# Kernel optimization log

Measured on AMD Instinct MI355X. Metric: run time of the kernel, lower is better.

The kernel has to match this reference:

```python
import jax, jax.numpy as jnp
import numpy as np

DIM = 128
B, N = 4, 4096


def setup_inputs() -> dict:
    key = jax.random.key(0)
    k1, k2, k3 = jax.random.split(key, 3)
    return {
        "key": jax.random.normal(k1, (B, N, DIM), dtype=jnp.float32),
        "query": jax.random.normal(k2, (B, N, DIM), dtype=jnp.float32),
        "value": jax.random.normal(k3, (B, N, DIM), dtype=jnp.float32),
    }


def reference(key, query, value):
    # score[b, i, j] = <query[b, i], key[b, j]> / sqrt(dim)
    inv_sqrt_dim = 1.0 / jnp.sqrt(jnp.float32(DIM))
    score = jnp.einsum("bqd,bkd->bqk", query, key) * inv_sqrt_dim
    attn = jax.nn.softmax(score, axis=-1)
    context = jnp.einsum("bqk,bkd->bqd", attn, value)
    return (context, attn)
```

## Files before the change

kernel.cpp:

```cpp
#include <hip/hip_runtime.h>
#include <hip/hip_bf16.h>

#define BDIM 4
#define NSEQ 4096
#define DHEAD 128
#define SCALE 0.08838834764831845f

typedef __bf16 bf16x8 __attribute__((ext_vector_type(8)));
typedef float f32x4 __attribute__((ext_vector_type(4)));
typedef float f32x16 __attribute__((ext_vector_type(16)));
typedef unsigned int u32x4 __attribute__((ext_vector_type(4)));

__device__ __forceinline__ unsigned short f2bf(float f){
    return __builtin_bit_cast(unsigned short, (__bf16)f);
}
__device__ __forceinline__ unsigned long long pack4(float4 u){
    return (unsigned long long)f2bf(u.x)
         | ((unsigned long long)f2bf(u.y) << 16)
         | ((unsigned long long)f2bf(u.z) << 32)
         | ((unsigned long long)f2bf(u.w) << 48);
}
__device__ __forceinline__ void gload_lds16(const void* g, void* l){
    __builtin_amdgcn_global_load_lds(
        (const __attribute__((address_space(1))) unsigned int*)g,
        (__attribute__((address_space(3))) unsigned int*)l, 16, 0, 0);
}

extern "C" __global__ __launch_bounds__(256, 4)
void attn_stats(const float* __restrict__ K, const float* __restrict__ Q,
                float* __restrict__ pbase, int pstride)
{
    __shared__ __align__(16) char Klds[64 * 256];

    const int bid = blockIdx.x;
    const int ks  = bid & 3;
    const int rt  = (bid >> 2) & 63;
    const int b   = bid >> 8;
    const int tid = threadIdx.x;
    const int lane = tid & 63;
    const int w    = tid >> 6;
    const int g    = lane >> 4;
    const int c    = lane & 15;
    const int rowbase = rt * 64;

    const float* qrow = Q + ((size_t)b * NSEQ + rowbase + w * 16 + c) * DHEAD;
    bf16x8 qf[4];
#pragma unroll
    for (int kk = 0; kk < 4; kk++) {
        const float4* p0 = (const float4*)(qrow + g * 8 + kk * 32);
        float4 u = p0[0], v = p0[1];
        bf16x8 t;
        t[0] = (__bf16)(u.x * SCALE); t[1] = (__bf16)(u.y * SCALE);
        t[2] = (__bf16)(u.z * SCALE); t[3] = (__bf16)(u.w * SCALE);
        t[4] = (__bf16)(v.x * SCALE); t[5] = (__bf16)(v.y * SCALE);
        t[6] = (__bf16)(v.z * SCALE); t[7] = (__bf16)(v.w * SCALE);
        qf[kk] = t;
    }

    float m[4], l[4];
#pragma unroll
    for (int r = 0; r < 4; r++) { m[r] = -1e30f; l[r] = 0.0f; }

    const int f  = tid & 31;
    const int r0 = tid >> 5;

    for (int kt = 0; kt < 16; kt++) {
        const float* ktile = K + ((size_t)b * NSEQ + ks * 1024 + kt * 64) * DHEAD;
#pragma unroll
        for (int i = 0; i < 8; i++) {
            int r = r0 + i * 8;
            float4 u = *(const float4*)(ktile + (size_t)r * DHEAD + f * 4);
            *(unsigned long long*)(Klds + r * 256 + ((f * 8) ^ ((r & 7) << 4))) = pack4(u);
        }
        __syncthreads();

        f32x4 acc[4];
#pragma unroll
        for (int n = 0; n < 4; n++) acc[n] = (f32x4){0.f, 0.f, 0.f, 0.f};
#pragma unroll
        for (int n = 0; n < 4; n++) {
            int row = n * 16 + c;
#pragma unroll
            for (int kk = 0; kk < 4; kk++) {
                bf16x8 kf = *(const bf16x8*)(Klds + row * 256 +
                                ((g * 16 + kk * 64) ^ ((row & 7) << 4)));
                acc[n] = __builtin_amdgcn_mfma_f32_16x16x32_bf16(qf[kk], kf, acc[n], 0, 0, 0);
            }
        }

#pragma unroll
        for (int r = 0; r < 4; r++) {
            float t = fmaxf(fmaxf(acc[0][r], acc[1][r]), fmaxf(acc[2][r], acc[3][r]));
            t = fmaxf(t, __shfl_xor(t, 1));
            t = fmaxf(t, __shfl_xor(t, 2));
            t = fmaxf(t, __shfl_xor(t, 4));
            t = fmaxf(t, __shfl_xor(t, 8));
            float mn = fmaxf(m[r], t);
            float sc = __expf(m[r] - mn);
            float ps = __expf(acc[0][r] - mn) + __expf(acc[1][r] - mn)
                     + __expf(acc[2][r] - mn) + __expf(acc[3][r] - mn);
            ps += __shfl_xor(ps, 1);
            ps += __shfl_xor(ps, 2);
            ps += __shfl_xor(ps, 4);
            ps += __shfl_xor(ps, 8);
            l[r] = l[r] * sc + ps;
            m[r] = mn;
        }
        __syncthreads();
    }

    if (c == 0) {
#pragma unroll
        for (int r = 0; r < 4; r++) {
            size_t row = rowbase + w * 16 + g * 4 + r;
            float* p = pbase + ((size_t)b * NSEQ + row) * pstride + ks * 2;
            p[0] = m[r];
            p[1] = l[r];
        }
    }
}

extern "C" __global__ __launch_bounds__(256, 4)
void repack3(const float* __restrict__ K, const float* __restrict__ V,
             char* __restrict__ ws)
{
    const int bid = blockIdx.x;
    const int T = bid & 127;
    const int b = bid >> 7;
    const int tid = threadIdx.x;

    char* Kp = ws + ((size_t)(b * 128 + T) << 14);
    const float* Ks = K + ((size_t)b * NSEQ + T * 32) * DHEAD;
    const float* Vs = V + ((size_t)b * NSEQ + T * 32) * DHEAD;

#pragma unroll
    for (int i = 0; i < 2; i++) {
        int u = tid + 256 * i;
        int ds = u >> 6, ln = u & 63;
        int m = ln & 31, hi = ln >> 5;
        const float* s = Ks + (size_t)m * DHEAD + ds * 16 + hi * 8;
        float4 a = *(const float4*)s;
        float4 bq = *(const float4*)(s + 4);
        ulonglong2 wv;
        wv.x = pack4(a);
        wv.y = pack4(bq);
        *(ulonglong2*)(Kp + u * 16) = wv;
    }
#pragma unroll
    for (int i = 0; i < 2; i++) {
        int u = tid + 256 * i;
        int f = u >> 6, ln = u & 63;
        int dg = f >> 1, kb = f & 1;
        int dd = ln & 31, hi = ln >> 5;
        int d = dg * 32 + dd;
        const float* s = Vs + (size_t)(kb * 16 + hi * 8) * DHEAD + d;
        float v0 = s[0 * DHEAD], v1 = s[1 * DHEAD], v2 = s[2 * DHEAD], v3 = s[3 * DHEAD];
        float v4 = s[4 * DHEAD], v5 = s[5 * DHEAD], v6 = s[6 * DHEAD], v7 = s[7 * DHEAD];
        ulonglong2 wv;
        wv.x = (unsigned long long)f2bf(v0)
             | ((unsigned long long)f2bf(v1) << 16)
             | ((unsigned long long)f2bf(v2) << 32)
             | ((unsigned long long)f2bf(v3) << 48);
        wv.y = (unsigned long long)f2bf(v4)
             | ((unsigned long long)f2bf(v5) << 16)
             | ((unsigned long long)f2bf(v6) << 32)
             | ((unsigned long long)f2bf(v7) << 48);
        *(ulonglong2*)(Kp + 8192 + u * 16) = wv;
    }
}

extern "C" __global__ __launch_bounds__(256, 2)
void attn_mf(const char* __restrict__ ws, const float* __restrict__ Q,
             float* __restrict__ out, float* __restrict__ part, int use_atomic)
{
    __shared__ __align__(16) char LDS[32768];

    const int bid = blockIdx.x;
    const int ks  = bid & 3;
    const int qt  = (bid >> 2) & 31;
    const int b   = bid >> 7;
    const int tid = threadIdx.x;
    const int wv  = tid >> 6;
    const int lane = tid & 63;
    const int hi   = lane >> 5;
    const int qq   = lane & 31;
    const int q    = qt * 128 + wv * 32 + qq;

    float* attn = out + (size_t)BDIM * NSEQ * DHEAD;
    const float* pb = (const float*)(ws + (8u << 20));

    float Cq;
    {
        const float* prow = pb + ((size_t)b * NSEQ + q) * 8;
        float4 p0 = *(const float4*)prow;
        float4 p1 = *(const float4*)(prow + 4);
        float M = fmaxf(fmaxf(p0.x, p0.z), fmaxf(p1.x, p1.z));
        float L = p0.y * __expf(p0.x - M) + p0.w * __expf(p0.z - M)
                + p1.y * __expf(p1.x - M) + p1.w * __expf(p1.z - M);
        Cq = M + __logf(L);
    }

    const float* qrow = Q + ((size_t)b * NSEQ + q) * DHEAD;
    bf16x8 qf[8];
#pragma unroll
    for (int ds = 0; ds < 8; ds++) {
        const float4* p0 = (const float4*)(qrow + ds * 16 + hi * 8);
        float4 u = p0[0], v = p0[1];
        bf16x8 t;
        t[0] = (__bf16)(u.x * SCALE); t[1] = (__bf16)(u.y * SCALE);
        t[2] = (__bf16)(u.z * SCALE); t[3] = (__bf16)(u.w * SCALE);
        t[4] = (__bf16)(v.x * SCALE); t[5] = (__bf16)(v.y * SCALE);
        t[6] = (__bf16)(v.z * SCALE); t[7] = (__bf16)(v.w * SCALE);
        qf[ds] = t;
    }

    f32x16 ctx[4];
#pragma unroll
    for (int dg = 0; dg < 4; dg++) ctx[dg] = (f32x16)(0.0f);

    const char* img = ws + ((size_t)(b * 128 + ks * 32) << 14);

#pragma unroll
    for (int i = 0; i < 4; i++) {
        int o = tid * 16 + i * 4096;
        gload_lds16(img + o, LDS + o);
    }

    float* arowb = attn + ((size_t)b * NSEQ + q) * NSEQ + ks * 1024 + 4 * hi;

    for (int kt = 0; kt < 32; kt++) {
        __builtin_amdgcn_s_barrier();
        __builtin_amdgcn_sched_barrier(0);
        if (kt < 31) {
            const char* src = img + ((size_t)(kt + 1) << 14);
            char* dst = LDS + (((kt + 1) & 1) << 14);
#pragma unroll
            for (int i = 0; i < 4; i++) {
                int o = tid * 16 + i * 4096;
                gload_lds16(src + o, dst + o);
            }
            asm volatile("s_waitcnt vmcnt(4)" ::: "memory");
        } else {
            asm volatile("s_waitcnt vmcnt(0)" ::: "memory");
        }
        __builtin_amdgcn_s_barrier();
        __builtin_amdgcn_sched_barrier(0);

        const char* bufc = LDS + ((kt & 1) << 14);

        f32x16 sacc = (f32x16)(0.0f);
        __builtin_amdgcn_s_setprio(1);
#pragma unroll
        for (int ds = 0; ds < 8; ds++) {
            bf16x8 kf = *(const bf16x8*)(bufc + ds * 1024 + lane * 16);
            sacc = __builtin_amdgcn_mfma_f32_32x32x16_bf16(kf, qf[ds], sacc, 0, 0, 0);
        }
        __builtin_amdgcn_s_setprio(0);

        float p[16];
#pragma unroll
        for (int r = 0; r < 16; r++) p[r] = __expf(sacc[r] - Cq);

        float* arow = arowb + kt * 32;
#pragma unroll
        for (int j = 0; j < 4; j++) {
            float4 pv = {p[4 * j], p[4 * j + 1], p[4 * j + 2], p[4 * j + 3]};
            *(float4*)(arow + 8 * j) = pv;
        }

        unsigned int bpk[8], sb[8];
#pragma unroll
        for (int i = 0; i < 8; i++)
            bpk[i] = (unsigned int)f2bf(p[2 * i]) | ((unsigned int)f2bf(p[2 * i + 1]) << 16);
#pragma unroll
        for (int i = 0; i < 8; i++)
            sb[i] = (unsigned int)__shfl_xor((int)bpk[i], 32);

        u32x4 w0, w1;
        w0[0] = hi ? sb[2] : bpk[0];
        w0[1] = hi ? sb[3] : bpk[1];
        w0[2] = hi ? bpk[2] : sb[0];
        w0[3] = hi ? bpk[3] : sb[1];
        w1[0] = hi ? sb[6] : bpk[4];
        w1[1] = hi ? sb[7] : bpk[5];
        w1[2] = hi ? bpk[6] : sb[4];
        w1[3] = hi ? bpk[7] : sb[5];
        bf16x8 pf0 = __builtin_bit_cast(bf16x8, w0);
        bf16x8 pf1 = __builtin_bit_cast(bf16x8, w1);

        __builtin_amdgcn_s_setprio(1);
#pragma unroll
        for (int dg = 0; dg < 4; dg++) {
            bf16x8 vf0 = *(const bf16x8*)(bufc + 8192 + (dg * 2 + 0) * 1024 + lane * 16);
            bf16x8 vf1 = *(const bf16x8*)(bufc + 8192 + (dg * 2 + 1) * 1024 + lane * 16);
            ctx[dg] = __builtin_amdgcn_mfma_f32_32x32x16_bf16(vf0, pf0, ctx[dg], 0, 0, 0);
            ctx[dg] = __builtin_amdgcn_mfma_f32_32x32x16_bf16(vf1, pf1, ctx[dg], 0, 0, 0);
        }
        __builtin_amdgcn_s_setprio(0);
    }

    if (!use_atomic) {
        float* cp = part + (((size_t)(ks * 4 + b) * NSEQ + q) * DHEAD) + 4 * hi;
#pragma unroll
        for (int dg = 0; dg < 4; dg++)
#pragma unroll
            for (int j = 0; j < 4; j++) {
                float4 v = {ctx[dg][4 * j], ctx[dg][4 * j + 1],
                            ctx[dg][4 * j + 2], ctx[dg][4 * j + 3]};
                *(float4*)(cp + dg * 32 + 8 * j) = v;
            }
    } else {
        float* cp = out + ((size_t)b * NSEQ + q) * DHEAD + 4 * hi;
#pragma unroll
        for (int dg = 0; dg < 4; dg++)
#pragma unroll
            for (int j = 0; j < 4; j++)
#pragma unroll
                for (int e = 0; e < 4; e++)
                    atomicAdd(cp + dg * 32 + 8 * j + e, ctx[dg][4 * j + e]);
    }
}

extern "C" __global__ __launch_bounds__(256, 4)
void ctx_reduce(const float4* __restrict__ part, float4* __restrict__ out)
{
    const size_t gt = (size_t)blockIdx.x * 256 + threadIdx.x;
    const size_t stride = (size_t)BDIM * NSEQ * DHEAD / 4;
    float4 a = part[gt];
    float4 b = part[gt + stride];
    float4 c = part[gt + 2 * stride];
    float4 d = part[gt + 3 * stride];
    float4 s;
    s.x = (a.x + b.x) + (c.x + d.x);
    s.y = (a.y + b.y) + (c.y + d.y);
    s.z = (a.z + b.z) + (c.z + d.z);
    s.w = (a.w + b.w) + (c.w + d.w);
    out[gt] = s;
}

extern "C" __global__ __launch_bounds__(512, 2)
void attn_final_fb(const float* __restrict__ K, const float* __restrict__ Q,
                   const float* __restrict__ V, float* __restrict__ out)
{
    __shared__ __align__(16) char LDS[81920];

    const int bid = blockIdx.x;
    const int rt  = bid & 63;
    const int b   = bid >> 6;
    const int tid = threadIdx.x;
    const int rowbase = rt * 64;
    const int lane = tid & 63;
    const int w    = tid >> 6;
    const int rw   = w & 3;
    const int grp  = w >> 2;
    const int g    = lane >> 4;
    const int c    = lane & 15;
    const int t    = tid & 255;

    float* ctxOut = out;
    float* attn   = out + (size_t)BDIM * NSEQ * DHEAD;

    char* Klds  = LDS + grp * 16384;
    char* Vtlds = LDS + 32768 + grp * 16384;
    char* Plds  = LDS + 65536 + w * 2048;

    float Cq;
    {
        const float* prow = attn + ((size_t)b * NSEQ + rowbase + rw * 16 + c) * NSEQ;
        float4 p0 = *(const float4*)prow;
        float4 p1 = *(const float4*)(prow + 4);
        float M = fmaxf(fmaxf(p0.x, p0.z), fmaxf(p1.x, p1.z));
        float L = p0.y * __expf(p0.x - M) + p0.w * __expf(p0.z - M)
                + p1.y * __expf(p1.x - M) + p1.w * __expf(p1.z - M);
        Cq = M + __logf(L);
    }

    const float* qrow = Q + ((size_t)b * NSEQ + rowbase + rw * 16 + c) * DHEAD;
    bf16x8 qf[4];
#pragma unroll
    for (int kk = 0; kk < 4; kk++) {
        const float4* p0 = (const float4*)(qrow + g * 8 + kk * 32);
        float4 u = p0[0], v = p0[1];
        bf16x8 tt;
        tt[0] = (__bf16)(u.x * SCALE); tt[1] = (__bf16)(u.y * SCALE);
        tt[2] = (__bf16)(u.z * SCALE); tt[3] = (__bf16)(u.w * SCALE);
        tt[4] = (__bf16)(v.x * SCALE); tt[5] = (__bf16)(v.y * SCALE);
        tt[6] = (__bf16)(v.z * SCALE); tt[7] = (__bf16)(v.w * SCALE);
        qf[kk] = tt;
    }

    f32x4 ctx[8];
#pragma unroll
    for (int n2 = 0; n2 < 8; n2++) ctx[n2] = (f32x4){0.f, 0.f, 0.f, 0.f};

    __syncthreads();

    const int fK = t & 31;
    const int rK = t >> 5;
    const int dq = t & 15;
    const int kb = t >> 4;
    const int k0 = kb * 4;
    const int d0 = dq * 2;

    const float* kbase = K + ((size_t)b * NSEQ + grp * 2048) * DHEAD;
    const float* vbase = V + ((size_t)b * NSEQ + grp * 2048) * DHEAD;

    float4 kreg[8];
    float2 vreg[4][4];

#pragma unroll
    for (int i = 0; i < 8; i++)
        kreg[i] = *(const float4*)(kbase + (size_t)(rK + i * 8) * DHEAD + fK * 4);
#pragma unroll
    for (int i = 0; i < 4; i++)
#pragma unroll
        for (int j = 0; j < 4; j++)
            vreg[i][j] = *(const float2*)(vbase + (size_t)(k0 + j) * DHEAD + d0 + 32 * i);

    for (int kt = 0; kt < 32; kt++) {
        __builtin_amdgcn_s_barrier();

#pragma unroll
        for (int i = 0; i < 8; i++) {
            int row = rK + i * 8;
            *(unsigned long long*)(Klds + row * 256 + ((fK * 8) ^ ((row & 7) << 4))) = pack4(kreg[i]);
        }
#pragma unroll
        for (int i = 0; i < 4; i++) {
            int d = d0 + 32 * i;
            unsigned long long rr0 =
                (unsigned long long)f2bf(vreg[i][0].x)
              | ((unsigned long long)f2bf(vreg[i][1].x) << 16)
              | ((unsigned long long)f2bf(vreg[i][2].x) << 32)
              | ((unsigned long long)f2bf(vreg[i][3].x) << 48);
            unsigned long long rr1 =
                (unsigned long long)f2bf(vreg[i][0].y)
              | ((unsigned long long)f2bf(vreg[i][1].y) << 16)
              | ((unsigned long long)f2bf(vreg[i][2].y) << 32)
              | ((unsigned long long)f2bf(vreg[i][3].y) << 48);
            int swz = (d & 7) << 4;
            *(unsigned long long*)(Vtlds + d * 128 + ((k0 * 2) ^ swz)) = rr0;
            *(unsigned long long*)(Vtlds + (d + 1) * 128 + ((k0 * 2) ^ (swz + 16))) = rr1;
        }
        asm volatile("s_waitcnt lgkmcnt(0)" ::: "memory");
        __builtin_amdgcn_s_barrier();

        {
            int kn = (kt + 1) & 31;
            const float* kp = kbase + (size_t)kn * 64 * DHEAD;
            const float* vp = vbase + (size_t)kn * 64 * DHEAD;
#pragma unroll
            for (int i = 0; i < 8; i++)
                kreg[i] = *(const float4*)(kp + (size_t)(rK + i * 8) * DHEAD + fK * 4);
#pragma unroll
            for (int i = 0; i < 4; i++)
#pragma unroll
                for (int j = 0; j < 4; j++)
                    vreg[i][j] = *(const float2*)(vp + (size_t)(k0 + j) * DHEAD + d0 + 32 * i);
        }

        f32x4 sacc[4];
#pragma unroll
        for (int nt = 0; nt < 4; nt++) sacc[nt] = (f32x4){0.f, 0.f, 0.f, 0.f};
        __builtin_amdgcn_s_setprio(1);
#pragma unroll
        for (int nt = 0; nt < 4; nt++) {
            int row = nt * 16 + c;
#pragma unroll
            for (int kk = 0; kk < 4; kk++) {
                bf16x8 kf = *(const bf16x8*)(Klds + row * 256 +
                                ((g * 16 + kk * 64) ^ ((row & 7) << 4)));
                sacc[nt] = __builtin_amdgcn_mfma_f32_16x16x32_bf16(kf, qf[kk], sacc[nt], 0, 0, 0);
            }
        }
        __builtin_amdgcn_s_setprio(0);

        const int col0 = grp * 2048 + kt * 64;
        float* arow = attn + ((size_t)b * NSEQ + rowbase + rw * 16 + c) * NSEQ + col0;
#pragma unroll
        for (int nt = 0; nt < 4; nt++) {
            float4 pv;
            pv.x = __expf(sacc[nt][0] - Cq);
            pv.y = __expf(sacc[nt][1] - Cq);
            pv.z = __expf(sacc[nt][2] - Cq);
            pv.w = __expf(sacc[nt][3] - Cq);
            *(float4*)(arow + nt * 16 + g * 4) = pv;
            *(unsigned long long*)(Plds + c * 128 +
                ((nt * 32 + g * 8) ^ ((c & 7) << 4))) = pack4(pv);
        }
        asm volatile("s_waitcnt lgkmcnt(0)" ::: "memory");
        __builtin_amdgcn_sched_barrier(0);

        bf16x8 pf[2];
#pragma unroll
        for (int kk = 0; kk < 2; kk++)
            pf[kk] = *(const bf16x8*)(Plds + c * 128 +
                        ((kk * 64 + g * 16) ^ ((c & 7) << 4)));

        __builtin_amdgcn_s_setprio(1);
#pragma unroll
        for (int n2 = 0; n2 < 8; n2++) {
            int d = n2 * 16 + c;
#pragma unroll
            for (int kk = 0; kk < 2; kk++) {
                bf16x8 vff = *(const bf16x8*)(Vtlds + d * 128 +
                                ((kk * 64 + g * 16) ^ ((d & 7) << 4)));
                ctx[n2] = __builtin_amdgcn_mfma_f32_16x16x32_bf16(pf[kk], vff, ctx[n2], 0, 0, 0);
            }
        }
        __builtin_amdgcn_s_setprio(0);
    }

    __syncthreads();

    float* red = (float*)LDS;
    if (grp == 1) {
#pragma unroll
        for (int n2 = 0; n2 < 8; n2++)
#pragma unroll
            for (int r = 0; r < 4; r++)
                red[(rw * 16 + g * 4 + r) * 128 + n2 * 16 + c] = ctx[n2][r];
    }
    __syncthreads();
    if (grp == 0) {
#pragma unroll
        for (int n2 = 0; n2 < 8; n2++)
#pragma unroll
            for (int r = 0; r < 4; r++) {
                size_t row = rowbase + rw * 16 + g * 4 + r;
                ctxOut[((size_t)b * NSEQ + row) * DHEAD + n2 * 16 + c] =
                    ctx[n2][r] + red[(rw * 16 + g * 4 + r) * 128 + n2 * 16 + c];
            }
    }
}

extern "C" void kernel_launch(void* const* d_in, const int* in_sizes, int n_in,
                              void* d_out, int out_size, void* d_ws, size_t ws_size,
                              hipStream_t stream)
{
    const float* K = (const float*)d_in[0];
    const float* Q = (const float*)d_in[1];
    const float* V = (const float*)d_in[2];
    float* out  = (float*)d_out;
    float* attn = out + (size_t)BDIM * NSEQ * DHEAD;

    const size_t ctx_bytes  = (size_t)BDIM * NSEQ * DHEAD * sizeof(float);
    const size_t need_part  = (9u << 20) + 4 * ctx_bytes;
    const size_t need_atom  = (8u << 20) + (size_t)BDIM * NSEQ * 8 * sizeof(float);

    if (ws_size >= need_part) {
        char* ws = (char*)d_ws;
        float* pb = (float*)(ws + (8u << 20));
        float* part = (float*)(ws + (9u << 20));
        attn_stats<<<dim3(4 * 64 * 4), dim3(256), 0, stream>>>(K, Q, pb, 8);
        repack3<<<dim3(4 * 128), dim3(256), 0, stream>>>(K, V, ws);
        attn_mf<<<dim3(512), dim3(256), 0, stream>>>(ws, Q, out, part, 0);
        ctx_reduce<<<dim3(2048), dim3(256), 0, stream>>>((const float4*)part, (float4*)out);
    } else if (ws_size >= need_atom) {
        char* ws = (char*)d_ws;
        float* pb = (float*)(ws + (8u << 20));
        hipMemsetAsync(out, 0, ctx_bytes, stream);
        attn_stats<<<dim3(4 * 64 * 4), dim3(256), 0, stream>>>(K, Q, pb, 8);
        repack3<<<dim3(4 * 128), dim3(256), 0, stream>>>(K, V, ws);
        attn_mf<<<dim3(512), dim3(256), 0, stream>>>(ws, Q, out, out, 1);
    } else {
        attn_stats<<<dim3(4 * 64 * 4), dim3(256), 0, stream>>>(K, Q, attn, NSEQ);
        attn_final_fb<<<dim3(4 * 64), dim3(512), 0, stream>>>(K, Q, V, out);
    }
}
```

Baseline: 176.4 us.

## Split key dimension eight ways and dual-accumulate score MFMAs

The main attention kernel now splits each query tile's keys into 8 chunks instead of 4, launching 1024 blocks with a launch bound of 3 blocks per CU. This is meant to improve occupancy and latency hiding on the 256-CU device. The score MFMA chain is split into two independent accumulators to shorten the dependency chain. The partial-context reduction now sums 8 slices, which doubles the workspace and the reduction traffic, and the Q fragments are loaded twice as many times in total.

```diff
diff --git a/kernel.cpp b/kernel.cpp
--- a/kernel.cpp
+++ b/kernel.cpp
@@ -169,16 +169,16 @@
     }
 }
 
-extern "C" __global__ __launch_bounds__(256, 2)
-void attn_mf(const char* __restrict__ ws, const float* __restrict__ Q,
-             float* __restrict__ out, float* __restrict__ part, int use_atomic)
+extern "C" __global__ __launch_bounds__(256, 3)
+void attn_mf2(const char* __restrict__ ws, const float* __restrict__ Q,
+              float* __restrict__ out, float* __restrict__ part, int use_atomic)
 {
     __shared__ __align__(16) char LDS[32768];
 
     const int bid = blockIdx.x;
-    const int ks  = bid & 3;
-    const int qt  = (bid >> 2) & 31;
-    const int b   = bid >> 7;
+    const int ks  = bid & 7;
+    const int qt  = (bid >> 3) & 31;
+    const int b   = bid >> 8;
     const int tid = threadIdx.x;
     const int wv  = tid >> 6;
     const int lane = tid & 63;
@@ -218,7 +218,7 @@
 #pragma unroll
     for (int dg = 0; dg < 4; dg++) ctx[dg] = (f32x16)(0.0f);
 
-    const char* img = ws + ((size_t)(b * 128 + ks * 32) << 14);
+    const char* img = ws + ((size_t)(b * 128 + ks * 16) << 14);
 
 #pragma unroll
     for (int i = 0; i < 4; i++) {
@@ -226,12 +226,12 @@
         gload_lds16(img + o, LDS + o);
     }
 
-    float* arowb = attn + ((size_t)b * NSEQ + q) * NSEQ + ks * 1024 + 4 * hi;
-
-    for (int kt = 0; kt < 32; kt++) {
+    float* arowb = attn + ((size_t)b * NSEQ + q) * NSEQ + ks * 512 + 4 * hi;
+
+    for (int kt = 0; kt < 16; kt++) {
         __builtin_amdgcn_s_barrier();
         __builtin_amdgcn_sched_barrier(0);
-        if (kt < 31) {
+        if (kt < 15) {
             const char* src = img + ((size_t)(kt + 1) << 14);
             char* dst = LDS + (((kt + 1) & 1) << 14);
 #pragma unroll
@@ -248,18 +248,20 @@
 
         const char* bufc = LDS + ((kt & 1) << 14);
 
-        f32x16 sacc = (f32x16)(0.0f);
+        f32x16 s0 = (f32x16)(0.0f), s1 = (f32x16)(0.0f);
         __builtin_amdgcn_s_setprio(1);
 #pragma unroll
-        for (int ds = 0; ds < 8; ds++) {
-            bf16x8 kf = *(const bf16x8*)(bufc + ds * 1024 + lane * 16);
-            sacc = __builtin_amdgcn_mfma_f32_32x32x16_bf16(kf, qf[ds], sacc, 0, 0, 0);
+        for (int dp = 0; dp < 4; dp++) {
+            bf16x8 kfa = *(const bf16x8*)(bufc + (2 * dp) * 1024 + lane * 16);
+            bf16x8 kfb = *(const bf16x8*)(bufc + (2 * dp + 1) * 1024 + lane * 16);
+            s0 = __builtin_amdgcn_mfma_f32_32x32x16_bf16(kfa, qf[2 * dp], s0, 0, 0, 0);
+            s1 = __builtin_amdgcn_mfma_f32_32x32x16_bf16(kfb, qf[2 * dp + 1], s1, 0, 0, 0);
         }
         __builtin_amdgcn_s_setprio(0);
 
         float p[16];
 #pragma unroll
-        for (int r = 0; r < 16; r++) p[r] = __expf(sacc[r] - Cq);
+        for (int r = 0; r < 16; r++) p[r] = __expf((s0[r] + s1[r]) - Cq);
 
         float* arow = arowb + kt * 32;
 #pragma unroll
@@ -322,19 +324,16 @@
 }
 
 extern "C" __global__ __launch_bounds__(256, 4)
-void ctx_reduce(const float4* __restrict__ part, float4* __restrict__ out)
+void ctx_reduce8(const float4* __restrict__ part, float4* __restrict__ out)
 {
     const size_t gt = (size_t)blockIdx.x * 256 + threadIdx.x;
     const size_t stride = (size_t)BDIM * NSEQ * DHEAD / 4;
-    float4 a = part[gt];
-    float4 b = part[gt + stride];
-    float4 c = part[gt + 2 * stride];
-    float4 d = part[gt + 3 * stride];
-    float4 s;
-    s.x = (a.x + b.x) + (c.x + d.x);
-    s.y = (a.y + b.y) + (c.y + d.y);
-    s.z = (a.z + b.z) + (c.z + d.z);
-    s.w = (a.w + b.w) + (c.w + d.w);
+    float4 s = part[gt];
+#pragma unroll
+    for (int i = 1; i < 8; i++) {
+        float4 a = part[gt + (size_t)i * stride];
+        s.x += a.x; s.y += a.y; s.z += a.z; s.w += a.w;
+    }
     out[gt] = s;
 }
 
@@ -545,8 +544,8 @@
     float* attn = out + (size_t)BDIM * NSEQ * DHEAD;
 
     const size_t ctx_bytes  = (size_t)BDIM * NSEQ * DHEAD * sizeof(float);
-    const size_t need_part  = (9u << 20) + 4 * ctx_bytes;
-    const size_t need_atom  = (8u << 20) + (size_t)BDIM * NSEQ * 8 * sizeof(float);
+    const size_t need_part  = (9u << 20) + 8 * ctx_bytes;
+    const size_t need_atom  = (9u << 20);
 
     if (ws_size >= need_part) {
         char* ws = (char*)d_ws;
@@ -554,15 +553,15 @@
         float* part = (float*)(ws + (9u << 20));
         attn_stats<<<dim3(4 * 64 * 4), dim3(256), 0, stream>>>(K, Q, pb, 8);
         repack3<<<dim3(4 * 128), dim3(256), 0, stream>>>(K, V, ws);
-        attn_mf<<<dim3(512), dim3(256), 0, stream>>>(ws, Q, out, part, 0);
-        ctx_reduce<<<dim3(2048), dim3(256), 0, stream>>>((const float4*)part, (float4*)out);
+        attn_mf2<<<dim3(1024), dim3(256), 0, stream>>>(ws, Q, out, part, 0);
+        ctx_reduce8<<<dim3(2048), dim3(256), 0, stream>>>((const float4*)part, (float4*)out);
     } else if (ws_size >= need_atom) {
         char* ws = (char*)d_ws;
         float* pb = (float*)(ws + (8u << 20));
         hipMemsetAsync(out, 0, ctx_bytes, stream);
         attn_stats<<<dim3(4 * 64 * 4), dim3(256), 0, stream>>>(K, Q, pb, 8);
         repack3<<<dim3(4 * 128), dim3(256), 0, stream>>>(K, V, ws);
-        attn_mf<<<dim3(512), dim3(256), 0, stream>>>(ws, Q, out, out, 1);
+        attn_mf2<<<dim3(1024), dim3(256), 0, stream>>>(ws, Q, out, out, 1);
     } else {
         attn_stats<<<dim3(4 * 64 * 4), dim3(256), 0, stream>>>(K, Q, attn, NSEQ);
         attn_final_fb<<<dim3(4 * 64), dim3(512), 0, stream>>>(K, Q, V, out);
```

Result: faster. 162.7 us (-7.8%).
